# Optimization experiments

Hardware: AMD Instinct MI355X
Metric: run time of the kernel (lower is better)

## Reference

```python
import jax, jax.numpy as jnp
import numpy as np

EMB = 1024
HEAD = 64

def setup_inputs() -> dict:
    key = jax.random.key(0)
    kx, kq, kk, kv = jax.random.split(key, 4)
    x = jax.random.normal(kx, (8, 2048, EMB), dtype=jnp.float32)
    # nn.Linear(emb, head, bias=False): y = x @ W.T, W: [head, emb]. Store as [emb, head].
    s = 1.0 / np.sqrt(EMB)
    Wq = jax.random.uniform(kq, (EMB, HEAD), jnp.float32, -s, s)
    Wk = jax.random.uniform(kk, (EMB, HEAD), jnp.float32, -s, s)
    Wv = jax.random.uniform(kv, (EMB, HEAD), jnp.float32, -s, s)
    return {"x": x, "Wq": Wq, "Wk": Wk, "Wv": Wv}

def reference(x, Wq, Wk, Wv):
    B, T, C = x.shape
    q = x @ Wq  # [B,T,H]
    k = x @ Wk
    v = x @ Wv
    # NOTE: original scales by emb_size C, not head_size.
    wei = jnp.einsum('bth,bsh->bts', q, k) / jnp.sqrt(jnp.asarray(C, x.dtype))
    causal = jnp.tril(jnp.ones((T, T), dtype=bool))
    wei = jnp.where(causal, wei, -jnp.inf)
    wei = jax.nn.softmax(wei, axis=-1)
    return jnp.einsum('bts,bsh->bth', wei, v)
```

## Files before the change

kernel.cpp:

```cpp
#include <hip/hip_runtime.h>
#include <hip/hip_bf16.h>

typedef __bf16 bf16_t;
typedef __bf16 bf16x8 __attribute__((ext_vector_type(8)));
typedef __bf16 bf16x4 __attribute__((ext_vector_type(4)));
typedef float  f32x4  __attribute__((ext_vector_type(4)));

#define MFMA_BF16(A, B, C) __builtin_amdgcn_mfma_f32_16x16x32_bf16((A), (B), (C), 0, 0, 0)

#define BATCH 8
#define SEQ   2048
#define EMB   1024
#define HEAD  64

typedef __attribute__((address_space(3))) void as3_void;
typedef const __attribute__((address_space(1))) void as1_void;
#define GLOAD_LDS16(g, l) \
  __builtin_amdgcn_global_load_lds((as1_void*)(g), (as3_void*)(l), 16, 0, 0)

__global__ __launch_bounds__(256) void wtrans_kernel(
    const float* __restrict__ Wq, const float* __restrict__ Wk,
    const float* __restrict__ Wv, bf16_t* __restrict__ WT)
{
  __shared__ float tile[64][65];
  const int m  = blockIdx.x >> 4;
  const int kt = blockIdx.x & 15;
  const float* W = (m == 0) ? Wq : (m == 1) ? Wk : Wv;
  const float scale = (m == 0) ? 0.045084219f : 1.0f;
  const int k0 = kt * 64;

  #pragma unroll
  for (int i = 0; i < 16; ++i) {
    int idx = i * 256 + threadIdx.x;
    int kk = idx >> 6, n = idx & 63;
    tile[kk][n] = W[(size_t)(k0 + kk) * HEAD + n];
  }
  __syncthreads();
  #pragma unroll
  for (int i = 0; i < 16; ++i) {
    int idx = i * 256 + threadIdx.x;
    int n = idx >> 6, kk = idx & 63;
    WT[((size_t)m * HEAD + n) * EMB + k0 + kk] = (bf16_t)(tile[kk][n] * scale);
  }
}

#define A_BYTES 16384
#define B_BYTES 24576
#define BUF_BYTES 40960

__global__ __launch_bounds__(512, 1) void qkv_kernel(
    const float* __restrict__ x, const bf16_t* __restrict__ WT,
    bf16_t* __restrict__ qo, bf16_t* __restrict__ ko, bf16_t* __restrict__ vT)
{
  __shared__ char lds[4 * BUF_BYTES];

  const int tid  = threadIdx.x;
  const int lane = tid & 63;
  const int wave = tid >> 6;
  const int l15 = lane & 15, l4 = lane >> 4;
  const int wm = wave >> 2, wn = wave & 3;
  const int rowbase = blockIdx.x * 64;
  const int phase = (blockIdx.x >> 3) & 15;

  const int a_rsub = lane >> 4;
  const int b_rsub = lane >> 3;
  const int b_koff = ((lane & 7) * 16) ^ (b_rsub << 4);

  const int aswz = (l15 & 7) << 5;
  const int bswz = (l15 & 7) << 4;

  f32x4 acc[2][3];
  #pragma unroll
  for (int m = 0; m < 2; ++m)
    #pragma unroll
    for (int n = 0; n < 3; ++n) acc[m][n] = (f32x4){0.f, 0.f, 0.f, 0.f};

#define STAGE(t)                                                               \
  {                                                                            \
    char* buf = lds + ((t) & 3) * BUF_BYTES;                                   \
    const int tp = ((t) + phase) & 15;                                         \
    _Pragma("unroll")                                                          \
    for (int j = 0; j < 2; ++j) {                                              \
      const int g = 2 * wave + j;                                              \
      const int koff = (l15 * 16) ^ ((((j) << 2) | a_rsub) << 5);              \
      const char* src = (const char*)x + (size_t)(rowbase + 4 * g + a_rsub)    \
                        * 4096 + (size_t)tp * 256 + koff;                      \
      GLOAD_LDS16(src, buf + g * 1024);                                        \
    }                                                                          \
    _Pragma("unroll")                                                          \
    for (int j = 0; j < 3; ++j) {                                              \
      const int g = 3 * wave + j;                                              \
      const char* src = (const char*)WT + (size_t)(8 * g + b_rsub) * 2048      \
                        + (size_t)tp * 128 + b_koff;                           \
      GLOAD_LDS16(src, buf + A_BYTES + g * 1024);                              \
    }                                                                          \
  }

#define COMPUTE(t)                                                             \
  {                                                                            \
    const char* Ab = lds + ((t) & 3) * BUF_BYTES;                              \
    const char* Bb = Ab + A_BYTES;                                             \
    _Pragma("unroll")                                                          \
    for (int ks = 0; ks < 2; ++ks) {                                           \
      bf16x8 afr[2];                                                           \
      _Pragma("unroll")                                                        \
      for (int m = 0; m < 2; ++m) {                                            \
        const int R = wm * 32 + m * 16 + l15;                                  \
        const char* rp = Ab + R * 256 + ((ks * 128 + l4 * 32) ^ aswz);         \
        f32x4 p0 = *(const f32x4*)(rp);                                        \
        f32x4 p1 = *(const f32x4*)(rp + 16);                                   \
        bf16x8 a;                                                              \
        a[0] = (bf16_t)p0.x; a[1] = (bf16_t)p0.y;                              \
        a[2] = (bf16_t)p0.z; a[3] = (bf16_t)p0.w;                              \
        a[4] = (bf16_t)p1.x; a[5] = (bf16_t)p1.y;                              \
        a[6] = (bf16_t)p1.z; a[7] = (bf16_t)p1.w;                              \
        afr[m] = a;                                                            \
      }                                                                        \
      _Pragma("unroll")                                                       \
      for (int n = 0; n < 3; ++n) {                                            \
        const int Rb = wn * 48 + n * 16 + l15;                                 \
        bf16x8 b = *(const bf16x8*)(Bb + Rb * 128 + ((ks * 64 + l4 * 16) ^ bswz)); \
        acc[0][n] = MFMA_BF16(afr[0], b, acc[0][n]);                           \
        acc[1][n] = MFMA_BF16(afr[1], b, acc[1][n]);                           \
      }                                                                        \
    }                                                                          \
  }

  STAGE(0); STAGE(1); STAGE(2);
  asm volatile("s_waitcnt vmcnt(10)" ::: "memory");
  __builtin_amdgcn_s_barrier();

  for (int t = 0; t < 13; ++t) {
    COMPUTE(t);
    STAGE(t + 3);
    asm volatile("s_waitcnt vmcnt(10)" ::: "memory");
    __builtin_amdgcn_s_barrier();
  }
  COMPUTE(13);
  asm volatile("s_waitcnt vmcnt(5)" ::: "memory");
  __builtin_amdgcn_s_barrier();
  COMPUTE(14);
  asm volatile("s_waitcnt vmcnt(0)" ::: "memory");
  __builtin_amdgcn_s_barrier();
  COMPUTE(15);
#undef STAGE
#undef COMPUTE

  #pragma unroll
  for (int n = 0; n < 3; ++n) {
    const int col = wn * 48 + n * 16;
    #pragma unroll
    for (int m = 0; m < 2; ++m) {
      const int r0 = rowbase + wm * 32 + m * 16 + l4 * 4;
      if (col < 64) {
        #pragma unroll
        for (int i = 0; i < 4; ++i)
          qo[(size_t)(r0 + i) * HEAD + col + l15] = (bf16_t)acc[m][n][i];
      } else if (col < 128) {
        #pragma unroll
        for (int i = 0; i < 4; ++i)
          ko[(size_t)(r0 + i) * HEAD + col - 64 + l15] = (bf16_t)acc[m][n][i];
      } else {
        const int h = col - 128 + l15;
        bf16x4 pk;
        #pragma unroll
        for (int i = 0; i < 4; ++i) pk[i] = (bf16_t)acc[m][n][i];
        *(bf16x4*)(vT + ((size_t)(r0 >> 11) * HEAD + h) * SEQ + (r0 & 2047)) = pk;
      }
    }
  }
}

__global__ __launch_bounds__(512, 2) void attn_kernel(
    const bf16_t* __restrict__ q, const bf16_t* __restrict__ k,
    const bf16_t* __restrict__ vT, float* __restrict__ out)
{
  __shared__ bf16_t P[8][16][72];
  __shared__ float olds[8][16][68];
  __shared__ float lsums[8][16];
  const int lane = threadIdx.x & 63;
  const int wave = threadIdx.x >> 6;
  const int l15 = lane & 15, l4 = lane >> 4;
  const int batch = blockIdx.x & 7;
  const int pair  = blockIdx.x >> 3;
  const int stripA = pair, stripB = 127 - pair;
  const int nA = (stripA >> 2) + 1;
  const int nB = (stripB >> 2) + 1;
  const int ntot = nA + nB;

  const bf16_t* kb = k  + (size_t)batch * SEQ * HEAD;
  const bf16_t* vb = vT + (size_t)batch * HEAD * SEQ;
  const bf16_t* qbA = q + ((size_t)batch * SEQ + stripA * 16) * HEAD;
  const bf16_t* qbB = q + ((size_t)batch * SEQ + stripB * 16) * HEAD;

  const bf16x8 aqA0 = *(const bf16x8*)(qbA + (size_t)l15 * HEAD + l4 * 8);
  const bf16x8 aqA1 = *(const bf16x8*)(qbA + (size_t)l15 * HEAD + 32 + l4 * 8);
  const bf16x8 aqB0 = *(const bf16x8*)(qbB + (size_t)l15 * HEAD + l4 * 8);
  const bf16x8 aqB1 = *(const bf16x8*)(qbB + (size_t)l15 * HEAD + 32 + l4 * 8);

  f32x4 oA[4], oB[4];
  #pragma unroll
  for (int i = 0; i < 4; ++i) {
    oA[i] = (f32x4){0.f, 0.f, 0.f, 0.f};
    oB[i] = (f32x4){0.f, 0.f, 0.f, 0.f};
  }
  float lsA[4] = {0.f, 0.f, 0.f, 0.f};
  float lsB[4] = {0.f, 0.f, 0.f, 0.f};

  for (int i = wave; i < ntot; i += 8) {
    const bool isA = (i < nA);
    const int tile = isA ? i : (i - nA);
    const int nS   = isA ? nA : nB;
    const int qrow = (isA ? stripA : stripB) * 16;
    const int kv0  = tile * 64;
    const bf16x8 aq0 = isA ? aqA0 : aqB0;
    const bf16x8 aq1 = isA ? aqA1 : aqB1;

    f32x4 s[4];
    #pragma unroll
    for (int nf = 0; nf < 4; ++nf) s[nf] = (f32x4){0.f, 0.f, 0.f, 0.f};
    __builtin_amdgcn_s_setprio(1);
    #pragma unroll
    for (int nf = 0; nf < 4; ++nf) {
      const bf16_t* kp = kb + (size_t)(kv0 + nf * 16 + l15) * HEAD + l4 * 8;
      bf16x8 b0 = *(const bf16x8*)kp;
      bf16x8 b1 = *(const bf16x8*)(kp + 32);
      s[nf] = MFMA_BF16(aq0, b0, s[nf]);
      s[nf] = MFMA_BF16(aq1, b1, s[nf]);
    }
    __builtin_amdgcn_s_setprio(0);

    const bool diag = (tile == nS - 1);
    float tsum[4] = {0.f, 0.f, 0.f, 0.f};
    #pragma unroll
    for (int nf = 0; nf < 4; ++nf) {
      #pragma unroll
      for (int i2 = 0; i2 < 4; ++i2) {
        float e = exp2f(s[nf][i2]);
        if (diag) {
          const int col = kv0 + nf * 16 + l15;
          const int row = qrow + l4 * 4 + i2;
          e = (col <= row) ? e : 0.f;
        }
        tsum[i2] += e;
        P[wave][l4 * 4 + i2][nf * 16 + l15] = (bf16_t)e;
      }
    }

    bf16x8 v0[4], v1[4];
    #pragma unroll
    for (int nf = 0; nf < 4; ++nf) {
      const bf16_t* vp = vb + (size_t)(nf * 16 + l15) * SEQ + kv0 + l4 * 8;
      v0[nf] = *(const bf16x8*)vp;
      v1[nf] = *(const bf16x8*)(vp + 32);
    }
    asm volatile("s_waitcnt lgkmcnt(0)" ::: "memory");

    bf16x8 ap0 = *(const bf16x8*)&P[wave][l15][l4 * 8];
    bf16x8 ap1 = *(const bf16x8*)&P[wave][l15][32 + l4 * 8];
    __builtin_amdgcn_s_setprio(1);
    if (isA) {
      #pragma unroll
      for (int nf = 0; nf < 4; ++nf) {
        oA[nf] = MFMA_BF16(ap0, v0[nf], oA[nf]);
        oA[nf] = MFMA_BF16(ap1, v1[nf], oA[nf]);
      }
      #pragma unroll
      for (int i2 = 0; i2 < 4; ++i2) lsA[i2] += tsum[i2];
    } else {
      #pragma unroll
      for (int nf = 0; nf < 4; ++nf) {
        oB[nf] = MFMA_BF16(ap0, v0[nf], oB[nf]);
        oB[nf] = MFMA_BF16(ap1, v1[nf], oB[nf]);
      }
      #pragma unroll
      for (int i2 = 0; i2 < 4; ++i2) lsB[i2] += tsum[i2];
    }
    __builtin_amdgcn_s_setprio(0);
  }

  #pragma unroll
  for (int pass = 0; pass < 2; ++pass) {
    #pragma unroll
    for (int i = 0; i < 4; ++i) {
      float v = pass == 0 ? lsA[i] : lsB[i];
      v += __shfl_xor(v, 1);
      v += __shfl_xor(v, 2);
      v += __shfl_xor(v, 4);
      v += __shfl_xor(v, 8);
      if (l15 == 0) lsums[wave][l4 * 4 + i] = v;
    }
    #pragma unroll
    for (int nf = 0; nf < 4; ++nf)
      #pragma unroll
      for (int i = 0; i < 4; ++i)
        olds[wave][l4 * 4 + i][nf * 16 + l15] = pass == 0 ? oA[nf][i] : oB[nf][i];
    __syncthreads();

    if (threadIdx.x < 256) {
      const int r = threadIdx.x >> 4, c0 = threadIdx.x & 15;
      float sum = 0.f;
      #pragma unroll
      for (int w = 0; w < 8; ++w) sum += lsums[w][r];
      const float rinv = 1.0f / sum;
      const int strip = pass == 0 ? stripA : stripB;
      float* ob = out + ((size_t)batch * SEQ + strip * 16 + r) * HEAD;
      #pragma unroll
      for (int j = 0; j < 4; ++j) {
        const int c = c0 + 16 * j;
        float v = 0.f;
        #pragma unroll
        for (int w = 0; w < 8; ++w) v += olds[w][r][c];
        ob[c] = v * rinv;
      }
    }
    __syncthreads();
  }
}

extern "C" void kernel_launch(void* const* d_in, const int* in_sizes, int n_in,
                              void* d_out, int out_size, void* d_ws, size_t ws_size,
                              hipStream_t stream)
{
  const float* x  = (const float*)d_in[0];
  const float* Wq = (const float*)d_in[1];
  const float* Wk = (const float*)d_in[2];
  const float* Wv = (const float*)d_in[3];
  float* out = (float*)d_out;

  const size_t SZ_QKV = (size_t)BATCH * SEQ * HEAD * sizeof(bf16_t);
  if (ws_size < 3 * SZ_QKV + (size_t)192 * EMB * sizeof(bf16_t)) return;
  char* ws = (char*)d_ws;
  bf16_t* qo = (bf16_t*)(ws);
  bf16_t* ko = (bf16_t*)(ws + SZ_QKV);
  bf16_t* vT = (bf16_t*)(ws + 2 * SZ_QKV);
  bf16_t* WT = (bf16_t*)(ws + 3 * SZ_QKV);

  wtrans_kernel<<<dim3(48),  dim3(256), 0, stream>>>(Wq, Wk, Wv, WT);
  qkv_kernel  <<<dim3(256), dim3(512), 0, stream>>>(x, WT, qo, ko, vT);
  attn_kernel <<<dim3(512), dim3(512), 0, stream>>>(qo, ko, vT, out);
}
```

Measured before the change: 58.64 us.

## Share K/V tiles across two adjacent query strips per wave in attention

Each attention block now covers 32 contiguous query rows of one batch with 4 waves, where it previously covered two mirrored 16-row strips with 8 waves. Each wave loads a K and V tile once and uses it for both 16-row halves, halving K/V global traffic per query row. Blocks are issued longest-first (descending causal length) to replace the mirrored-pair load balancing, and the final cross-wave reduction now sums 4 partials instead of 8. The trade-off is more register pressure per wave (two sets of scores) and fewer waves per block to hide latency.

```diff
diff --git a/kernel.cpp b/kernel.cpp
--- a/kernel.cpp
+++ b/kernel.cpp
@@ -116,7 +116,7 @@
         a[6] = (bf16_t)p1.z; a[7] = (bf16_t)p1.w;                              \
         afr[m] = a;                                                            \
       }                                                                        \
-      _Pragma("unroll")                                                       \
+      _Pragma("unroll")                                                        \
       for (int n = 0; n < 3; ++n) {                                            \
         const int Rb = wn * 48 + n * 16 + l15;                                 \
         bf16x8 b = *(const bf16x8*)(Bb + Rb * 128 + ((ks * 64 + l4 * 16) ^ bswz)); \
@@ -171,27 +171,26 @@
   }
 }
 
-__global__ __launch_bounds__(512, 2) void attn_kernel(
+__global__ __launch_bounds__(256) void attn_kernel(
     const bf16_t* __restrict__ q, const bf16_t* __restrict__ k,
     const bf16_t* __restrict__ vT, float* __restrict__ out)
 {
-  __shared__ bf16_t P[8][16][72];
-  __shared__ float olds[8][16][68];
-  __shared__ float lsums[8][16];
+  __shared__ bf16_t P[4][16][72];
+  __shared__ float olds[4][16][68];
+  __shared__ float lsums[4][16];
   const int lane = threadIdx.x & 63;
   const int wave = threadIdx.x >> 6;
   const int l15 = lane & 15, l4 = lane >> 4;
   const int batch = blockIdx.x & 7;
-  const int pair  = blockIdx.x >> 3;
-  const int stripA = pair, stripB = 127 - pair;
-  const int nA = (stripA >> 2) + 1;
-  const int nB = (stripB >> 2) + 1;
-  const int ntot = nA + nB;
+  const int u = 63 - (int)(blockIdx.x >> 3);
+  const int qrowA = u * 32;
+  const int qrowB = u * 32 + 16;
+  const int ntiles = (u >> 1) + 1;
 
   const bf16_t* kb = k  + (size_t)batch * SEQ * HEAD;
   const bf16_t* vb = vT + (size_t)batch * HEAD * SEQ;
-  const bf16_t* qbA = q + ((size_t)batch * SEQ + stripA * 16) * HEAD;
-  const bf16_t* qbB = q + ((size_t)batch * SEQ + stripB * 16) * HEAD;
+  const bf16_t* qbA = q + ((size_t)batch * SEQ + qrowA) * HEAD;
+  const bf16_t* qbB = q + ((size_t)batch * SEQ + qrowB) * HEAD;
 
   const bf16x8 aqA0 = *(const bf16x8*)(qbA + (size_t)l15 * HEAD + l4 * 8);
   const bf16x8 aqA1 = *(const bf16x8*)(qbA + (size_t)l15 * HEAD + 32 + l4 * 8);
@@ -207,45 +206,27 @@
   float lsA[4] = {0.f, 0.f, 0.f, 0.f};
   float lsB[4] = {0.f, 0.f, 0.f, 0.f};
 
-  for (int i = wave; i < ntot; i += 8) {
-    const bool isA = (i < nA);
-    const int tile = isA ? i : (i - nA);
-    const int nS   = isA ? nA : nB;
-    const int qrow = (isA ? stripA : stripB) * 16;
-    const int kv0  = tile * 64;
-    const bf16x8 aq0 = isA ? aqA0 : aqB0;
-    const bf16x8 aq1 = isA ? aqA1 : aqB1;
-
-    f32x4 s[4];
-    #pragma unroll
-    for (int nf = 0; nf < 4; ++nf) s[nf] = (f32x4){0.f, 0.f, 0.f, 0.f};
+  for (int t = wave; t < ntiles; t += 4) {
+    const int kv0 = t * 64;
+
+    f32x4 sA[4], sB[4];
+    #pragma unroll
+    for (int nf = 0; nf < 4; ++nf) {
+      sA[nf] = (f32x4){0.f, 0.f, 0.f, 0.f};
+      sB[nf] = (f32x4){0.f, 0.f, 0.f, 0.f};
+    }
     __builtin_amdgcn_s_setprio(1);
     #pragma unroll
     for (int nf = 0; nf < 4; ++nf) {
       const bf16_t* kp = kb + (size_t)(kv0 + nf * 16 + l15) * HEAD + l4 * 8;
       bf16x8 b0 = *(const bf16x8*)kp;
       bf16x8 b1 = *(const bf16x8*)(kp + 32);
-      s[nf] = MFMA_BF16(aq0, b0, s[nf]);
-      s[nf] = MFMA_BF16(aq1, b1, s[nf]);
+      sA[nf] = MFMA_BF16(aqA0, b0, sA[nf]);
+      sB[nf] = MFMA_BF16(aqB0, b0, sB[nf]);
+      sA[nf] = MFMA_BF16(aqA1, b1, sA[nf]);
+      sB[nf] = MFMA_BF16(aqB1, b1, sB[nf]);
     }
     __builtin_amdgcn_s_setprio(0);
-
-    const bool diag = (tile == nS - 1);
-    float tsum[4] = {0.f, 0.f, 0.f, 0.f};
-    #pragma unroll
-    for (int nf = 0; nf < 4; ++nf) {
-      #pragma unroll
-      for (int i2 = 0; i2 < 4; ++i2) {
-        float e = exp2f(s[nf][i2]);
-        if (diag) {
-          const int col = kv0 + nf * 16 + l15;
-          const int row = qrow + l4 * 4 + i2;
-          e = (col <= row) ? e : 0.f;
-        }
-        tsum[i2] += e;
-        P[wave][l4 * 4 + i2][nf * 16 + l15] = (bf16_t)e;
-      }
-    }
 
     bf16x8 v0[4], v1[4];
     #pragma unroll
@@ -254,29 +235,66 @@
       v0[nf] = *(const bf16x8*)vp;
       v1[nf] = *(const bf16x8*)(vp + 32);
     }
-    asm volatile("s_waitcnt lgkmcnt(0)" ::: "memory");
-
-    bf16x8 ap0 = *(const bf16x8*)&P[wave][l15][l4 * 8];
-    bf16x8 ap1 = *(const bf16x8*)&P[wave][l15][32 + l4 * 8];
-    __builtin_amdgcn_s_setprio(1);
-    if (isA) {
+
+    const bool diag = (t == ntiles - 1);
+
+    {
+      float tsum[4] = {0.f, 0.f, 0.f, 0.f};
+      #pragma unroll
+      for (int nf = 0; nf < 4; ++nf) {
+        #pragma unroll
+        for (int i2 = 0; i2 < 4; ++i2) {
+          float e = exp2f(sA[nf][i2]);
+          if (diag) {
+            const int col = kv0 + nf * 16 + l15;
+            const int row = qrowA + l4 * 4 + i2;
+            e = (col <= row) ? e : 0.f;
+          }
+          tsum[i2] += e;
+          P[wave][l4 * 4 + i2][nf * 16 + l15] = (bf16_t)e;
+        }
+      }
+      bf16x8 ap0 = *(const bf16x8*)&P[wave][l15][l4 * 8];
+      bf16x8 ap1 = *(const bf16x8*)&P[wave][l15][32 + l4 * 8];
+      __builtin_amdgcn_s_setprio(1);
       #pragma unroll
       for (int nf = 0; nf < 4; ++nf) {
         oA[nf] = MFMA_BF16(ap0, v0[nf], oA[nf]);
         oA[nf] = MFMA_BF16(ap1, v1[nf], oA[nf]);
       }
+      __builtin_amdgcn_s_setprio(0);
       #pragma unroll
       for (int i2 = 0; i2 < 4; ++i2) lsA[i2] += tsum[i2];
-    } else {
+    }
+
+    {
+      float tsum[4] = {0.f, 0.f, 0.f, 0.f};
+      #pragma unroll
+      for (int nf = 0; nf < 4; ++nf) {
+        #pragma unroll
+        for (int i2 = 0; i2 < 4; ++i2) {
+          float e = exp2f(sB[nf][i2]);
+          if (diag) {
+            const int col = kv0 + nf * 16 + l15;
+            const int row = qrowB + l4 * 4 + i2;
+            e = (col <= row) ? e : 0.f;
+          }
+          tsum[i2] += e;
+          P[wave][l4 * 4 + i2][nf * 16 + l15] = (bf16_t)e;
+        }
+      }
+      bf16x8 ap0 = *(const bf16x8*)&P[wave][l15][l4 * 8];
+      bf16x8 ap1 = *(const bf16x8*)&P[wave][l15][32 + l4 * 8];
+      __builtin_amdgcn_s_setprio(1);
       #pragma unroll
       for (int nf = 0; nf < 4; ++nf) {
         oB[nf] = MFMA_BF16(ap0, v0[nf], oB[nf]);
         oB[nf] = MFMA_BF16(ap1, v1[nf], oB[nf]);
       }
+      __builtin_amdgcn_s_setprio(0);
       #pragma unroll
       for (int i2 = 0; i2 < 4; ++i2) lsB[i2] += tsum[i2];
     }
-    __builtin_amdgcn_s_setprio(0);
   }
 
   #pragma unroll
@@ -297,20 +315,16 @@
         olds[wave][l4 * 4 + i][nf * 16 + l15] = pass == 0 ? oA[nf][i] : oB[nf][i];
     __syncthreads();
 
-    if (threadIdx.x < 256) {
+    {
       const int r = threadIdx.x >> 4, c0 = threadIdx.x & 15;
-      float sum = 0.f;
-      #pragma unroll
-      for (int w = 0; w < 8; ++w) sum += lsums[w][r];
+      const float sum = lsums[0][r] + lsums[1][r] + lsums[2][r] + lsums[3][r];
       const float rinv = 1.0f / sum;
-      const int strip = pass == 0 ? stripA : stripB;
-      float* ob = out + ((size_t)batch * SEQ + strip * 16 + r) * HEAD;
+      const int qrow = pass == 0 ? qrowA : qrowB;
+      float* ob = out + ((size_t)batch * SEQ + qrow + r) * HEAD;
       #pragma unroll
       for (int j = 0; j < 4; ++j) {
         const int c = c0 + 16 * j;
-        float v = 0.f;
-        #pragma unroll
-        for (int w = 0; w < 8; ++w) v += olds[w][r][c];
+        float v = olds[0][r][c] + olds[1][r][c] + olds[2][r][c] + olds[3][r][c];
         ob[c] = v * rinv;
       }
     }
@@ -338,5 +352,5 @@
 
   wtrans_kernel<<<dim3(48),  dim3(256), 0, stream>>>(Wq, Wk, Wv, WT);
   qkv_kernel  <<<dim3(256), dim3(512), 0, stream>>>(x, WT, qo, ko, vT);
-  attn_kernel <<<dim3(512), dim3(512), 0, stream>>>(qo, ko, vT, out);
+  attn_kernel <<<dim3(512), dim3(256), 0, stream>>>(qo, ko, vT, out);
 }
```

Result: faster. 51.03 us (-13.0%).
